# Performance work log

Hardware: AMD Instinct MI355X
Metric: run time of the kernel (lower is better)

Reference implementation:

```python
import jax, jax.numpy as jnp
import numpy as np

B, S, E, H = 4, 4096, 512, 64


def setup_inputs() -> dict:
    key = jax.random.key(0)
    ks = jax.random.split(key, 6)
    query = jax.random.normal(ks[0], (B, S, E), dtype=jnp.float32)
    key_t = jax.random.normal(ks[1], (B, S, E), dtype=jnp.float32)
    value = jax.random.normal(ks[2], (B, S, E), dtype=jnp.float32)
    # nn.Linear weights are [out, in] = [H, E]; biases [H]
    Wq = jax.random.normal(ks[3], (H, E), dtype=jnp.float32) * 0.02
    Wk = jax.random.normal(ks[4], (H, E), dtype=jnp.float32) * 0.02
    Wv = jax.random.normal(ks[5], (H, E), dtype=jnp.float32) * 0.02
    bq = jnp.zeros((H,), jnp.float32)
    bk = jnp.zeros((H,), jnp.float32)
    bv = jnp.zeros((H,), jnp.float32)
    # causal mask, broadcast over batch; masked_fill where mask == 0
    mask = jnp.tril(jnp.ones((1, S, S), dtype=jnp.bool_))
    return {"query": query, "key": key_t, "value": value,
            "Wq": Wq, "bq": bq, "Wk": Wk, "bk": bk, "Wv": Wv, "bv": bv,
            "mask": mask}


def reference(query, key, value, Wq, bq, Wk, bk, Wv, bv, mask):
    # Bug-faithful: d_k is the LAST dim of the *input* query, i.e. embed_dim
    d_k = query.shape[-1]
    q = jnp.einsum('bse,he->bsh', query, Wq) + bq   # [B,S,H]
    k = jnp.einsum('bse,he->bsh', key, Wk) + bk     # [B,S,H]
    v = jnp.einsum('bse,he->bsh', value, Wv) + bv   # [B,S,H]
    scores = jnp.einsum('bqh,bkh->bqk', q, k) / jnp.sqrt(jnp.float32(d_k))  # [B,S,S]
    scores = jnp.where(mask, scores, -jnp.inf)
    weights = jax.nn.softmax(scores, axis=-1)
    # dropout_rate = 0.0 -> Dropout is identity
    out = jnp.einsum('bqk,bkh->bqh', weights, v)    # [B,S,H]
    return out
```

## Files before the change

### kernel.cpp

```cpp
#include <hip/hip_runtime.h>
#include <hip/hip_bf16.h>
#include <math.h>

typedef unsigned short u16;
typedef unsigned int   u32;
typedef __attribute__((ext_vector_type(8)))  short bf16x8_t;
typedef __attribute__((ext_vector_type(4)))  float f32x4_t;
typedef __attribute__((ext_vector_type(16))) float f32x16_t;
typedef __attribute__((ext_vector_type(4)))  int   i32x4_t;
typedef __attribute__((ext_vector_type(2)))  u32   u32x2_t;

#define SEQ 4096
#define EMB 512
#define HD  64
#define NBATCH 4
#define C2 0.063758718f

#define NPAIR 136
#define SLOTS (NBATCH * NPAIR * 8)

__device__ __forceinline__ u16 to_bf(float f) {
    __hip_bfloat16 h = __float2bfloat16(f);
    return __builtin_bit_cast(u16, h);
}

__device__ __forceinline__ void stage16(const void* g, void* l) {
    __builtin_amdgcn_global_load_lds(
        (const __attribute__((address_space(1))) void*)g,
        (__attribute__((address_space(3))) void*)l, 16, 0, 0);
}

__global__ __launch_bounds__(256)
void wprep_kernel(const float* __restrict__ Wq, const float* __restrict__ Wk,
                  const float* __restrict__ Wv, u16* __restrict__ wbf)
{
    const int zkt = blockIdx.x;
    const int z   = zkt >> 4;
    const int kt  = zkt & 15;
    const float* W = (z == 0) ? Wq : (z == 1) ? Wk : Wv;
    const int kn   = threadIdx.x >> 6;
    const int lane = threadIdx.x & 63;
    const int l15  = lane & 15;
    const int lg   = lane >> 4;

    const float* src = W + (size_t)(kn * 16 + l15) * EMB + kt * 32 + lg * 8;
    f32x4_t f0 = *reinterpret_cast<const f32x4_t*>(src);
    f32x4_t f1 = *reinterpret_cast<const f32x4_t*>(src + 4);
    u16 tmp[8];
    #pragma unroll
    for (int e = 0; e < 4; ++e) { tmp[e] = to_bf(f0[e]); tmp[4 + e] = to_bf(f1[e]); }
    *reinterpret_cast<i32x4_t*>(
        &wbf[((size_t)((z * 16 + kt) * 4 + kn)) * 512 + lane * 8]) =
        *reinterpret_cast<const i32x4_t*>(tmp);
}

__global__ __launch_bounds__(256)
void proj_kernel(const float* __restrict__ q_in, const float* __restrict__ k_in,
                 const float* __restrict__ v_in, const u16* __restrict__ wbf,
                 const float* __restrict__ bq, const float* __restrict__ bk,
                 const float* __restrict__ bv,
                 u16* __restrict__ outQ, u16* __restrict__ outK,
                 u16* __restrict__ outVT)
{
    const int z = blockIdx.y;
    const float* in   = (z == 0) ? q_in : (z == 1) ? k_in : v_in;
    const float* bias = (z == 0) ? bq   : (z == 1) ? bk   : bv;

    __shared__ __align__(16) float A_lds[4][4][16][32];

    const int tid  = threadIdx.x;
    const int lane = tid & 63;
    const int w    = tid >> 6;
    const int l15  = lane & 15;
    const int lg   = lane >> 4;
    const int g0   = blockIdx.x * 64;

    const u16* wz = wbf + (size_t)z * 16 * 4 * 512 + lane * 8;

    float bvals[4];
    #pragma unroll
    for (int kn = 0; kn < 4; ++kn) bvals[kn] = bias[kn * 16 + l15];
    asm volatile("" :: "v"(bvals[0]), "v"(bvals[1]), "v"(bvals[2]), "v"(bvals[3]));

    const int sr = lane >> 3;
    const int sc = (lane & 7) ^ (sr & 7);
    const float* abase = in + (size_t)(g0 + w * 16 + sr) * EMB + sc * 4;

#define ISSUE(kt)                                                               \
    {                                                                           \
        stage16(abase +            (kt) * 32, &A_lds[(kt) & 3][w][0][0]);       \
        stage16(abase + 8 * EMB +  (kt) * 32, &A_lds[(kt) & 3][w][8][0]);       \
    }

    f32x4_t acc[4];
    #pragma unroll
    for (int i = 0; i < 4; ++i)
        #pragma unroll
        for (int j = 0; j < 4; ++j) acc[i][j] = 0.f;

    const int rsw = l15 & 7;
    const int p0  = (lg * 2) ^ rsw;

    ISSUE(0); ISSUE(1); ISSUE(2); ISSUE(3);

    #pragma unroll
    for (int kt = 0; kt < 16; ++kt) {
        if (kt <= 12)      asm volatile("s_waitcnt vmcnt(6)" ::: "memory");
        else if (kt == 13) asm volatile("s_waitcnt vmcnt(4)" ::: "memory");
        else if (kt == 14) asm volatile("s_waitcnt vmcnt(2)" ::: "memory");
        else               asm volatile("s_waitcnt vmcnt(0)" ::: "memory");
        __builtin_amdgcn_sched_barrier(0);

        const int s = kt & 3;
        f32x4_t a0 = *reinterpret_cast<const f32x4_t*>(&A_lds[s][w][l15][p0 * 4]);
        f32x4_t a1 = *reinterpret_cast<const f32x4_t*>(&A_lds[s][w][l15][(p0 ^ 1) * 4]);
        u16 ta[8];
        #pragma unroll
        for (int e = 0; e < 4; ++e) { ta[e] = to_bf(a0[e]); ta[4 + e] = to_bf(a1[e]); }
        bf16x8_t af = *reinterpret_cast<const bf16x8_t*>(ta);
        #pragma unroll
        for (int kn = 0; kn < 4; ++kn) {
            bf16x8_t wfrag = *reinterpret_cast<const bf16x8_t*>(
                wz + ((size_t)(kt * 4 + kn) << 9));
            acc[kn] = __builtin_amdgcn_mfma_f32_16x16x32_bf16(af, wfrag, acc[kn], 0, 0, 0);
        }
        if (kt < 12) ISSUE(kt + 4);
    }
#undef ISSUE

    #pragma unroll
    for (int kn = 0; kn < 4; ++kn) {
        const int col = kn * 16 + l15;
        #pragma unroll
        for (int j = 0; j < 4; ++j) {
            const int grow = g0 + w * 16 + lg * 4 + j;
            const u16 val = to_bf(acc[kn][j] + bvals[kn]);
            if (z == 0) {
                outQ[(size_t)grow * HD + col] = val;
            } else if (z == 1) {
                outK[(size_t)grow * HD + col] = val;
            } else {
                const int b = grow >> 12, s2 = grow & (SEQ - 1);
                outVT[((size_t)(b * HD + col)) * SEQ + s2] = val;
            }
        }
    }
}

__global__ __launch_bounds__(512, 4)
void attn8_kernel(const u16* __restrict__ Q, const u16* __restrict__ K,
                  const u16* __restrict__ VT,
                  u16* __restrict__ partO, float* __restrict__ partL)
{
    __shared__ u16 Kt[2][64 * 64];
    __shared__ u16 Vt[2][64 * 64];
    __shared__ u16 Pt[8][32 * 64];

    const int tid  = threadIdx.x;
    const int w    = tid >> 6;
    const int lane = tid & 63;
    const int q31  = lane & 31;
    const int half = lane >> 5;

    const int b = blockIdx.y;
    const int y = blockIdx.x;
    int g = 0;
    while ((g + 1) * (g + 2) / 2 <= y) ++g;
    const int c = y - g * (g + 1) / 2;

    const int R0   = 256 * g + 32 * w;
    const int q_g  = R0 + q31;
    const int nt_w = 4 * g + (w >> 1) + 1;
    const int t0   = 4 * c, t1 = 4 * c + 4;

    const u16* Kb  = K  + (size_t)b * SEQ * HD;
    const u16* VTb = VT + (size_t)b * HD * SEQ;

    const int srow = w * 8 + (lane >> 3);
    const int schk = (lane & 7) ^ ((lane >> 3) & 7);

    bf16x8_t qf0, qf1, qf2, qf3;
    {
        const u16* qp = Q + ((size_t)b * SEQ + q_g) * HD + 8 * half;
        qf0 = *(const bf16x8_t*)(qp + 0);
        qf1 = *(const bf16x8_t*)(qp + 16);
        qf2 = *(const bf16x8_t*)(qp + 32);
        qf3 = *(const bf16x8_t*)(qp + 48);
    }

    f32x16_t acc0, acc1;
    #pragma unroll
    for (int i = 0; i < 16; ++i) { acc0[i] = 0.f; acc1[i] = 0.f; }
    float lsum = 0.f;

    auto STAGE = [&](int u, int t) {
        stage16(&Kb[((size_t)(t * 64 + srow)) * HD + schk * 8], &Kt[u][w * 512]);
        stage16(&VTb[(size_t)srow * SEQ + t * 64 + schk * 8],   &Vt[u][w * 512]);
    };

    STAGE(0, t0);
    asm volatile("s_waitcnt vmcnt(0)" ::: "memory");
    __syncthreads();

    for (int t = t0; t < t1; ++t) {
        const int u = (t - t0) & 1;
        if (t + 1 < t1) STAGE(u ^ 1, t + 1);
        if (t < nt_w) {
            const bool last = (t == nt_w - 1);
            #pragma unroll
            for (int ksub = 0; ksub < 2; ++ksub) {
                f32x16_t sf;
                #pragma unroll
                for (int i = 0; i < 16; ++i) sf[i] = 0.f;
                const int kl = ksub * 32 + q31;
                #pragma unroll
                for (int s = 0; s < 4; ++s) {
                    bf16x8_t a = *(const bf16x8_t*)
                        &Kt[u][kl * 64 + ((s * 16 + 8 * half) ^ ((kl & 7) << 3))];
                    bf16x8_t qq = (s == 0) ? qf0 : (s == 1) ? qf1 : (s == 2) ? qf2 : qf3;
                    sf = __builtin_amdgcn_mfma_f32_32x32x16_bf16(a, qq, sf, 0, 0, 0);
                }
                #pragma unroll
                for (int j = 0; j < 4; ++j) {
                    float p[4];
                    #pragma unroll
                    for (int e = 0; e < 4; ++e) {
                        const int kk    = 8 * j + 4 * half + e;
                        const int key_g = t * 64 + ksub * 32 + kk;
                        float v = exp2f(sf[4 * j + e] * C2);
                        if (last && key_g > q_g) v = 0.f;
                        lsum += v;
                        p[e] = v;
                    }
                    u32x2_t pk;
                    pk[0] = (u32)to_bf(p[0]) | ((u32)to_bf(p[1]) << 16);
                    pk[1] = (u32)to_bf(p[2]) | ((u32)to_bf(p[3]) << 16);
                    const int col = (ksub * 32 + 8 * j + 4 * half) ^ ((q31 & 7) << 3);
                    *(u32x2_t*)&Pt[w][q31 * 64 + col] = pk;
                }
            }
            asm volatile("s_waitcnt lgkmcnt(0)" ::: "memory");
            __builtin_amdgcn_sched_barrier(0);
            #pragma unroll
            for (int kp = 0; kp < 4; ++kp) {
                bf16x8_t pb = *(const bf16x8_t*)
                    &Pt[w][q31 * 64 + ((kp * 16 + 8 * half) ^ ((q31 & 7) << 3))];
                {
                    const int dl = q31;
                    bf16x8_t va = *(const bf16x8_t*)
                        &Vt[u][dl * 64 + ((kp * 16 + 8 * half) ^ ((dl & 7) << 3))];
                    acc0 = __builtin_amdgcn_mfma_f32_32x32x16_bf16(va, pb, acc0, 0, 0, 0);
                }
                {
                    const int dl = 32 + q31;
                    bf16x8_t va = *(const bf16x8_t*)
                        &Vt[u][dl * 64 + ((kp * 16 + 8 * half) ^ ((dl & 7) << 3))];
                    acc1 = __builtin_amdgcn_mfma_f32_32x32x16_bf16(va, pb, acc1, 0, 0, 0);
                }
            }
        }
        asm volatile("s_waitcnt vmcnt(0)" ::: "memory");
        __syncthreads();
    }

    lsum += __shfl_xor(lsum, 32);
    const int slot = (b * NPAIR + y) * 8 + w;
    u16* po = partO + (size_t)slot * 2048;
    #pragma unroll
    for (int dsub = 0; dsub < 2; ++dsub) {
        #pragma unroll
        for (int j = 0; j < 4; ++j) {
            const f32x16_t& a = dsub ? acc1 : acc0;
            u32x2_t pk;
            pk[0] = (u32)to_bf(a[4 * j + 0]) | ((u32)to_bf(a[4 * j + 1]) << 16);
            pk[1] = (u32)to_bf(a[4 * j + 2]) | ((u32)to_bf(a[4 * j + 3]) << 16);
            const int d = 32 * dsub + 8 * j + 4 * half;
            *(u32x2_t*)&po[q31 * 64 + d] = pk;
        }
    }
    if (half == 0) partL[(size_t)slot * 32 + q31] = lsum;
}

__global__ __launch_bounds__(256)
void reduce8_kernel(const u16* __restrict__ partO, const float* __restrict__ partL,
                    float* __restrict__ out)
{
    const int x  = blockIdx.x;
    const int b  = x >> 7;
    const int gw = x & 127;
    const int g  = gw >> 3;
    const int w  = gw & 7;
    const int ybase = g * (g + 1) / 2;

    const int t  = threadIdx.x;
    const int q  = t >> 3;
    const int d0 = (t & 7) * 8;

    float acc[8];
    #pragma unroll
    for (int i = 0; i < 8; ++i) acc[i] = 0.f;
    float l = 0.f;

    for (int c = 0; c <= g; ++c) {
        const int slot = (b * NPAIR + ybase + c) * 8 + w;
        i32x4_t raw = *(const i32x4_t*)(partO + (size_t)slot * 2048 + q * 64 + d0);
        const u16* pr = (const u16*)&raw;
        #pragma unroll
        for (int i = 0; i < 8; ++i) {
            u32 bits = ((u32)pr[i]) << 16;
            acc[i] += __builtin_bit_cast(float, bits);
        }
        l += partL[(size_t)slot * 32 + q];
    }
    const float inv = 1.f / l;
    f32x4_t r0, r1;
    #pragma unroll
    for (int i = 0; i < 4; ++i) { r0[i] = acc[i] * inv; r1[i] = acc[4 + i] * inv; }
    const size_t row = (size_t)b * SEQ + g * 256 + w * 32 + q;
    *(f32x4_t*)&out[row * HD + d0]     = r0;
    *(f32x4_t*)&out[row * HD + d0 + 4] = r1;
}

extern "C" void kernel_launch(void* const* d_in, const int* in_sizes, int n_in,
                              void* d_out, int out_size, void* d_ws, size_t ws_size,
                              hipStream_t stream)
{
    const float* q_in = (const float*)d_in[0];
    const float* k_in = (const float*)d_in[1];
    const float* v_in = (const float*)d_in[2];
    const float* Wq   = (const float*)d_in[3];
    const float* bq   = (const float*)d_in[4];
    const float* Wk   = (const float*)d_in[5];
    const float* bk   = (const float*)d_in[6];
    const float* Wv   = (const float*)d_in[7];
    const float* bv   = (const float*)d_in[8];
    float* out = (float*)d_out;

    const size_t NQ = (size_t)NBATCH * SEQ * HD;
    u16* wsQ   = (u16*)d_ws;
    u16* wsK   = wsQ + NQ;
    u16* wsVT  = wsK + NQ;
    u16* partO = wsVT + NQ;
    float* partL = (float*)(partO + (size_t)SLOTS * 2048);
    u16* wbf = partO;

    wprep_kernel<<<dim3(48), 256, 0, stream>>>(Wq, Wk, Wv, wbf);
    proj_kernel<<<dim3(256, 3), 256, 0, stream>>>(q_in, k_in, v_in, wbf,
                                                  bq, bk, bv, wsQ, wsK, wsVT);
    attn8_kernel<<<dim3(NPAIR, NBATCH), 512, 0, stream>>>(wsQ, wsK, wsVT, partO, partL);
    reduce8_kernel<<<dim3(512), 256, 0, stream>>>(partO, partL, out);
}
```

Measured before the change: 70.67 us.

## Stage projection weights in LDS and load activations directly to registers

The projection kernel now copies the whole bf16 weight slice for its z index (64KB) into LDS once per block. It loads each activation row's fp32 fragments straight from global memory into registers through inline global_load_dwordx4 with a 4-deep register ring, where before it staged activations through LDS and read weights from global. Blocks grow to 512 threads covering 128 rows, so the grid halves. The intent is to cut the global weight re-reads and the LDS traffic for activations. In exchange each block uses 64KB of LDS, which lowers occupancy, and the vmcnt wait counts must line up with the new staging loads.

```diff
diff --git a/kernel.cpp b/kernel.cpp
--- a/kernel.cpp
+++ b/kernel.cpp
@@ -54,7 +54,7 @@
         *reinterpret_cast<const i32x4_t*>(tmp);
 }
 
-__global__ __launch_bounds__(256)
+__global__ __launch_bounds__(512)
 void proj_kernel(const float* __restrict__ q_in, const float* __restrict__ k_in,
                  const float* __restrict__ v_in, const u16* __restrict__ wbf,
                  const float* __restrict__ bq, const float* __restrict__ bk,
@@ -66,42 +66,51 @@
     const float* in   = (z == 0) ? q_in : (z == 1) ? k_in : v_in;
     const float* bias = (z == 0) ? bq   : (z == 1) ? bk   : bv;
 
-    __shared__ __align__(16) float A_lds[4][4][16][32];
+    __shared__ __align__(16) u16 W_lds[64 * 512];
 
     const int tid  = threadIdx.x;
     const int lane = tid & 63;
     const int w    = tid >> 6;
     const int l15  = lane & 15;
     const int lg   = lane >> 4;
-    const int g0   = blockIdx.x * 64;
-
-    const u16* wz = wbf + (size_t)z * 16 * 4 * 512 + lane * 8;
+    const int g0   = blockIdx.x * 128;
 
     float bvals[4];
     #pragma unroll
     for (int kn = 0; kn < 4; ++kn) bvals[kn] = bias[kn * 16 + l15];
     asm volatile("" :: "v"(bvals[0]), "v"(bvals[1]), "v"(bvals[2]), "v"(bvals[3]));
 
-    const int sr = lane >> 3;
-    const int sc = (lane & 7) ^ (sr & 7);
-    const float* abase = in + (size_t)(g0 + w * 16 + sr) * EMB + sc * 4;
-
-#define ISSUE(kt)                                                               \
-    {                                                                           \
-        stage16(abase +            (kt) * 32, &A_lds[(kt) & 3][w][0][0]);       \
-        stage16(abase + 8 * EMB +  (kt) * 32, &A_lds[(kt) & 3][w][8][0]);       \
-    }
+    {
+        const u16* wsrc = wbf + (size_t)z * 32768;
+        #pragma unroll
+        for (int i = 0; i < 8; ++i)
+            stage16(wsrc + (size_t)(w * 8 + i) * 512 + lane * 8,
+                    &W_lds[(w * 8 + i) * 512]);
+    }
+
+    const int row = g0 + w * 16 + l15;
+    const float* arow = in + (size_t)row * EMB + lg * 8;
+
+    f32x4_t a0[4], a1[4];
+
+#define ISSUE(kt)                                                              \
+    asm volatile("global_load_dwordx4 %0, %2, off\n\t"                         \
+                 "global_load_dwordx4 %1, %2, off offset:16"                   \
+                 : "=&v"(a0[(kt) & 3]), "=&v"(a1[(kt) & 3])                    \
+                 : "v"(arow + (kt) * 32)                                       \
+                 : "memory");
+
+    ISSUE(0); ISSUE(1); ISSUE(2); ISSUE(3);
+
+    asm volatile("s_waitcnt vmcnt(8)" ::: "memory");
+    __builtin_amdgcn_s_barrier();
+    __builtin_amdgcn_sched_barrier(0);
 
     f32x4_t acc[4];
     #pragma unroll
     for (int i = 0; i < 4; ++i)
         #pragma unroll
         for (int j = 0; j < 4; ++j) acc[i][j] = 0.f;
-
-    const int rsw = l15 & 7;
-    const int p0  = (lg * 2) ^ rsw;
-
-    ISSUE(0); ISSUE(1); ISSUE(2); ISSUE(3);
 
     #pragma unroll
     for (int kt = 0; kt < 16; ++kt) {
@@ -112,16 +121,14 @@
         __builtin_amdgcn_sched_barrier(0);
 
         const int s = kt & 3;
-        f32x4_t a0 = *reinterpret_cast<const f32x4_t*>(&A_lds[s][w][l15][p0 * 4]);
-        f32x4_t a1 = *reinterpret_cast<const f32x4_t*>(&A_lds[s][w][l15][(p0 ^ 1) * 4]);
         u16 ta[8];
         #pragma unroll
-        for (int e = 0; e < 4; ++e) { ta[e] = to_bf(a0[e]); ta[4 + e] = to_bf(a1[e]); }
+        for (int e = 0; e < 4; ++e) { ta[e] = to_bf(a0[s][e]); ta[4 + e] = to_bf(a1[s][e]); }
         bf16x8_t af = *reinterpret_cast<const bf16x8_t*>(ta);
         #pragma unroll
         for (int kn = 0; kn < 4; ++kn) {
             bf16x8_t wfrag = *reinterpret_cast<const bf16x8_t*>(
-                wz + ((size_t)(kt * 4 + kn) << 9));
+                &W_lds[(size_t)(kt * 4 + kn) * 512 + lane * 8]);
             acc[kn] = __builtin_amdgcn_mfma_f32_16x16x32_bf16(af, wfrag, acc[kn], 0, 0, 0);
         }
         if (kt < 12) ISSUE(kt + 4);
@@ -345,7 +352,7 @@
     u16* wbf = partO;
 
     wprep_kernel<<<dim3(48), 256, 0, stream>>>(Wq, Wk, Wv, wbf);
-    proj_kernel<<<dim3(256, 3), 256, 0, stream>>>(q_in, k_in, v_in, wbf,
+    proj_kernel<<<dim3(128, 3), 512, 0, stream>>>(q_in, k_in, v_in, wbf,
                                                   bq, bk, bv, wsQ, wsK, wsVT);
     attn8_kernel<<<dim3(NPAIR, NBATCH), 512, 0, stream>>>(wsQ, wsK, wsVT, partO, partL);
     reduce8_kernel<<<dim3(512), 256, 0, stream>>>(partO, partL, out);
```

Result: slower. 73.92 us (+4.6%).
